# Optimization experiments

Hardware: AMD Instinct MI355X
Metric: run time of the kernel (lower is better)

The kernel has to match this reference:

```python
import jax, jax.numpy as jnp
import numpy as np

WZ, WH, WW = 2, 6, 12  # window_size (Z, H, W)
NUM_HEADS = 6


def _layernorm(x, g, b, eps=1e-5):
    m = jnp.mean(x, axis=-1, keepdims=True)
    v = jnp.mean((x - m) ** 2, axis=-1, keepdims=True)
    return (x - m) * jax.lax.rsqrt(v + eps) * g + b


def setup_inputs() -> dict:
    key = jax.random.key(0)
    ks = jax.random.split(key, 8)
    B, Z, H, W, C = 1, 8, 91, 180, 192
    s = 0.02
    return {
        "x": jax.random.normal(ks[0], (B, Z * H * W, C), jnp.float32),
        "norm1_g": jnp.ones((C,), jnp.float32),
        "norm1_b": jnp.zeros((C,), jnp.float32),
        "qkv_w": jax.random.normal(ks[1], (3 * C, C), jnp.float32) * s,
        "qkv_b": jnp.zeros((3 * C,), jnp.float32),
        "proj_w": jax.random.normal(ks[2], (C, C), jnp.float32) * s,
        "proj_b": jnp.zeros((C,), jnp.float32),
        "norm2_g": jnp.ones((C,), jnp.float32),
        "norm2_b": jnp.zeros((C,), jnp.float32),
        "fc1_w": jax.random.normal(ks[3], (4 * C, C), jnp.float32) * s,
        "fc1_b": jnp.zeros((4 * C,), jnp.float32),
        "fc2_w": jax.random.normal(ks[4], (C, 4 * C), jnp.float32) * s,
        "fc2_b": jnp.zeros((C,), jnp.float32),
        "Z": Z, "H": H, "W": W, "roll": 1,
    }


def _forward(x, norm1_g, norm1_b, qkv_w, qkv_b, proj_w, proj_b,
             norm2_g, norm2_b, fc1_w, fc1_b, fc2_w, fc2_b, Z, H, W, roll):
    B, N, C = x.shape
    shortcut = x
    x = x.reshape(B, Z, H, W, C)
    # pad to window multiples (right-pad, as in torch F.pad)
    pz, ph, pw = (-Z) % WZ, (-H) % WH, (-W) % WW
    x = jnp.pad(x, ((0, 0), (0, pz), (0, ph), (0, pw), (0, 0)))
    Zp, Hp, Wp = Z + pz, H + ph, W + pw
    if roll:
        x = jnp.roll(x, (-(WZ // 2), -(WH // 2), -(WW // 2)), axis=(1, 2, 3))
    # window partition -> (B*nW, wz*wh*ww, C)
    x = x.reshape(B, Zp // WZ, WZ, Hp // WH, WH, Wp // WW, WW, C)
    x = x.transpose(0, 1, 3, 5, 2, 4, 6, 7).reshape(-1, WZ * WH * WW, C)
    xw = _layernorm(x, norm1_g, norm1_b)
    # windowed multi-head attention (mask is always None in this module)
    nw, L, _ = xw.shape
    hd = C // NUM_HEADS
    qkv = (xw @ qkv_w.T + qkv_b).reshape(nw, L, 3, NUM_HEADS, hd)
    q, k, v = jnp.moveaxis(qkv, 2, 0)        # each (nw, L, nh, hd)
    q = q * (hd ** -0.5)
    attn = jnp.einsum('nqhd,nkhd->nhqk', q, k)
    attn = jax.nn.softmax(attn, axis=-1)
    out = jnp.einsum('nhqk,nkhd->nqhd', attn, v).reshape(nw, L, C)
    out = out @ proj_w.T + proj_b
    # window reverse
    x = out.reshape(B, Zp // WZ, Hp // WH, Wp // WW, WZ, WH, WW, C)
    x = x.transpose(0, 1, 4, 2, 5, 3, 6, 7).reshape(B, Zp, Hp, Wp, C)
    if roll:
        x = jnp.roll(x, (WZ // 2, WH // 2, WW // 2), axis=(1, 2, 3))
    x = x[:, :Z, :H, :W, :].reshape(B, Z * H * W, C)
    x = shortcut + x
    # MLP with post-norm (as written in the source: x + norm2(mlp(x)))
    h = jax.nn.gelu(x @ fc1_w.T + fc1_b, approximate=False)
    h = h @ fc2_w.T + fc2_b
    return x + _layernorm(h, norm2_g, norm2_b)


def reference(x, norm1_g, norm1_b, qkv_w, qkv_b, proj_w, proj_b,
              norm2_g, norm2_b, fc1_w, fc1_b, fc2_w, fc2_b, Z, H, W, roll):
    return _forward(x, norm1_g, norm1_b, qkv_w, qkv_b, proj_w, proj_b,
                    norm2_g, norm2_b, fc1_w, fc1_b, fc2_w, fc2_b, Z, H, W, roll)
```

## Files before the change

kernel.cpp:

```cpp
#include <hip/hip_runtime.h>
#include <hip/hip_bf16.h>
#include <math.h>

#define C_DIM 192
#define NH 6
#define HD 32
#define L_WIN 144
#define NWIN 960
#define MROWS (NWIN * L_WIN)
#define NTOK 131040
#define Z_ 8
#define H_ 91
#define W_ 180
#define HP_ 96
#define WS_REQUIRED 212336640ull

#define OFF_WBF   0ull
#define OFF_XWC   1048576ull
#define OFF_QKVB  51367936ull
#define OFF_ATTNO 1048576ull
#define OFF_X1B   51367936ull
#define WO_QKV  0
#define WO_PROJ 110592
#define WO_FC1  147456
#define WO_FC2  294912
#define WO_BETA 442368
#define W_TOTAL 442560

typedef __attribute__((ext_vector_type(8))) short bf16x8;
typedef __attribute__((ext_vector_type(4))) short s16x4;
typedef __attribute__((ext_vector_type(4))) float f32x4;

__device__ __forceinline__ short f2bf(float f) {
    union { __hip_bfloat16 h; short s; } u; u.h = __float2bfloat16(f); return u.s;
}
__device__ __forceinline__ float bf2f(short s) {
    return __uint_as_float(((unsigned int)(unsigned short)s) << 16);
}

__device__ __forceinline__ int win_token_to_tok(int r) {
    int n = r / L_WIN, l = r - n * L_WIN;
    int wz = n / 240;
    int rem = n - wz * 240;
    int wh = rem / 15;
    int ww = rem - wh * 15;
    int iz = l / 72;
    int r2 = l - iz * 72;
    int ih = r2 / 12;
    int iw = r2 - ih * 12;
    int z = wz * 2 + iz;
    int h = wh * 6 + ih;
    int w = ww * 12 + iw;
    int zp = z + 1; if (zp >= Z_) zp -= Z_;
    int hp = h + 3; if (hp >= HP_) hp -= HP_;
    int wp = w + 6; if (wp >= W_) wp -= W_;
    if (hp >= H_) return -1;
    return (zp * H_ + hp) * W_ + wp;
}

__global__ __launch_bounds__(256)
void wconv_kernel(const float* __restrict__ qw, const float* __restrict__ pw,
                  const float* __restrict__ f1w, const float* __restrict__ f2w,
                  const float* __restrict__ n1b, short* __restrict__ wbf) {
    int i = blockIdx.x * 256 + threadIdx.x;
    if (i >= W_TOTAL) return;
    float v;
    if (i < WO_PROJ)      v = qw[i];
    else if (i < WO_FC1)  v = pw[i - WO_PROJ];
    else if (i < WO_FC2)  v = f1w[i - WO_FC1];
    else if (i < WO_BETA) v = f2w[i - WO_FC2];
    else                  v = n1b[i - WO_BETA];
    wbf[i] = f2bf(v);
}

__global__ __launch_bounds__(256)
void ln_tok_kernel(const float* __restrict__ x, const float* __restrict__ g,
                   const float* __restrict__ b, short* __restrict__ xwc) {
    int wave = threadIdx.x >> 6, lane = threadIdx.x & 63;
    int r = blockIdx.x * 4 + wave;
    if (r >= NTOK) return;
    const float* p = x + (size_t)r * C_DIM;
    float v0 = p[lane], v1 = p[lane + 64], v2 = p[lane + 128];
    float s = v0 + v1 + v2;
    float sq = v0 * v0 + v1 * v1 + v2 * v2;
    #pragma unroll
    for (int off = 32; off; off >>= 1) {
        s += __shfl_xor(s, off);
        sq += __shfl_xor(sq, off);
    }
    float m = s * (1.f / 192.f);
    float var = sq * (1.f / 192.f) - m * m;
    float inv = rsqrtf(var + 1e-5f);
    short* o = xwc + (size_t)r * C_DIM;
    o[lane]       = f2bf((v0 - m) * inv * g[lane]       + b[lane]);
    o[lane + 64]  = f2bf((v1 - m) * inv * g[lane + 64]  + b[lane + 64]);
    o[lane + 128] = f2bf((v2 - m) * inv * g[lane + 128] + b[lane + 128]);
}

__global__ __launch_bounds__(256)
void qkv_gemm(const short* __restrict__ xwc, const short* __restrict__ wq,
              const short* __restrict__ beta, const float* __restrict__ bias,
              short* __restrict__ qkvb) {
    __shared__ __align__(16) short As[128][200];
    int t = threadIdx.x, w = t >> 6, l = t & 63, g = l >> 4, c = l & 15;
    int bid = blockIdx.x + 9 * blockIdx.y;
    int xcd = bid & 7, sq_ = bid >> 3;
    int bx = sq_ % 9, by = xcd + 8 * (sq_ / 9);
    int row0 = by * 128, col0 = bx * 64;
    int wr = (w >> 1) * 64, wc = (w & 1) * 32;
    const short* wqb = wq + (size_t)(col0 + wc + c) * 192 + g * 8;
    bf16x8 wv[6][2];
    #pragma unroll
    for (int ks = 0; ks < 6; ks++)
        #pragma unroll
        for (int n = 0; n < 2; n++)
            wv[ks][n] = *(const bf16x8*)(wqb + n * 3072 + ks * 32);
    {
        int r = t & 127;
        int th = t >> 7;
        int tok = win_token_to_tok(row0 + r);
        const short* src = (tok >= 0) ? xwc + (size_t)tok * C_DIM : beta;
        #pragma unroll
        for (int i = 0; i < 12; i++) {
            int cidx = th + 2 * i;
            *(bf16x8*)(&As[r][cidx * 8]) = *(const bf16x8*)(src + cidx * 8);
        }
    }
    __syncthreads();
    f32x4 acc[4][2] = {};
    #pragma unroll
    for (int ks = 0; ks < 6; ks++) {
        bf16x8 af[4];
        #pragma unroll
        for (int m = 0; m < 4; m++)
            af[m] = *(const bf16x8*)(&As[wr + 16 * m + c][ks * 32 + g * 8]);
        #pragma unroll
        for (int m = 0; m < 4; m++)
            #pragma unroll
            for (int n = 0; n < 2; n++)
                acc[m][n] = __builtin_amdgcn_mfma_f32_16x16x32_bf16(af[m], wv[ks][n], acc[m][n], 0, 0, 0);
    }
    #pragma unroll
    for (int m = 0; m < 4; m++)
        #pragma unroll
        for (int reg = 0; reg < 4; reg++) {
            int r = row0 + wr + 16 * m + 4 * g + reg;
            int win = r / 144, ll = r - win * 144;
            #pragma unroll
            for (int n = 0; n < 2; n++) {
                int col = col0 + wc + 16 * n + c;
                int sec = col / 192;
                int head = (col - sec * 192) >> 5;
                int d = col & 31;
                size_t dst = ((size_t)(win * 6 + head) * 3 + sec) * 4608 + ll * 32 + d;
                qkvb[dst] = f2bf(acc[m][n][reg] + bias[col]);
            }
        }
}

__global__ __launch_bounds__(192)
void attn_mfma(const short* __restrict__ qkvb, short* __restrict__ attno) {
    __shared__ __align__(16) short Vt[32][168];
    __shared__ __align__(16) short Pl[3][16][168];
    int blk = blockIdx.x;
    int win = blk / NH, head = blk - win * NH;
    int t = threadIdx.x, w = t >> 6, l = t & 63, g = l >> 4, c = l & 15;
    const short* qb = qkvb + (size_t)(win * 6 + head) * 13824;
    const short* kb = qb + 4608;
    const short* vb = qb + 9216;
    for (int ch = t; ch < 576; ch += 192) {
        int kv = ch >> 2, cc = (ch & 3) * 8;
        bf16x8 v = *(const bf16x8*)(vb + kv * 32 + cc);
        #pragma unroll
        for (int j = 0; j < 8; j++) Vt[cc + j][kv] = v[j];
    }
    for (int i = t; i < 32 * 24; i += 192) Vt[i / 24][144 + i % 24] = 0;
    for (int i = l; i < 16 * 24; i += 64) Pl[w][i / 24][144 + i % 24] = 0;
    __syncthreads();

    bf16x8 kf[9];
    #pragma unroll
    for (int n = 0; n < 9; n++)
        kf[n] = *(const bf16x8*)(kb + (16 * n + c) * 32 + g * 8);

    const float scale2 = 0.2550348668f;
    for (int m = w; m < 9; m += 3) {
        bf16x8 qf = *(const bf16x8*)(qb + (16 * m + c) * 32 + g * 8);
        f32x4 sv[9];
        #pragma unroll
        for (int n = 0; n < 9; n++) {
            f32x4 z = {};
            sv[n] = __builtin_amdgcn_mfma_f32_16x16x32_bf16(qf, kf[n], z, 0, 0, 0);
        }
        float mx[4], rs[4];
        #pragma unroll
        for (int reg = 0; reg < 4; reg++) {
            float v = -1e30f;
            #pragma unroll
            for (int n = 0; n < 9; n++) { sv[n][reg] *= scale2; v = fmaxf(v, sv[n][reg]); }
            #pragma unroll
            for (int off = 1; off <= 8; off <<= 1) v = fmaxf(v, __shfl_xor(v, off));
            mx[reg] = v;
        }
        #pragma unroll
        for (int reg = 0; reg < 4; reg++) {
            float acc = 0.f;
            #pragma unroll
            for (int n = 0; n < 9; n++) {
                float e = exp2f(sv[n][reg] - mx[reg]);
                sv[n][reg] = e;
                acc += e;
            }
            #pragma unroll
            for (int off = 1; off <= 8; off <<= 1) acc += __shfl_xor(acc, off);
            rs[reg] = 1.f / acc;
        }
        #pragma unroll
        for (int n = 0; n < 9; n++)
            #pragma unroll
            for (int reg = 0; reg < 4; reg++)
                Pl[w][4 * g + reg][16 * n + c] = f2bf(sv[n][reg]);
        asm volatile("s_waitcnt lgkmcnt(0)" ::: "memory");
        f32x4 o[2] = {};
        #pragma unroll
        for (int ks = 0; ks < 5; ks++) {
            bf16x8 pa = *(const bf16x8*)(&Pl[w][c][32 * ks + 8 * g]);
            #pragma unroll
            for (int df = 0; df < 2; df++) {
                bf16x8 vv = *(const bf16x8*)(&Vt[16 * df + c][32 * ks + 8 * g]);
                o[df] = __builtin_amdgcn_mfma_f32_16x16x32_bf16(pa, vv, o[df], 0, 0, 0);
            }
        }
        #pragma unroll
        for (int reg = 0; reg < 4; reg++) {
            int grow = win * L_WIN + 16 * m + 4 * g + reg;
            int tok = win_token_to_tok(grow);
            if (tok < 0) continue;
            #pragma unroll
            for (int df = 0; df < 2; df++)
                attno[(size_t)tok * C_DIM + head * HD + 16 * df + c] =
                    f2bf(o[df][reg] * rs[reg]);
        }
    }
}

__global__ __launch_bounds__(256)
void proj_gemm(const short* __restrict__ attno, const short* __restrict__ wp,
               const float* __restrict__ bias, const float* __restrict__ x,
               short* __restrict__ x1b) {
    __shared__ __align__(16) short As[128][200];
    int t = threadIdx.x, w = t >> 6, l = t & 63, g = l >> 4, c = l & 15;
    int bid = blockIdx.x + 3 * blockIdx.y;
    int xcd = bid & 7, sq_ = bid >> 3;
    int bx = sq_ % 3, by = xcd + 8 * (sq_ / 3);
    int row0 = by * 128, col0 = bx * 64;
    int wr = (w >> 1) * 64, wc = (w & 1) * 32;
    const short* wpb = wp + (size_t)(col0 + wc + c) * 192 + g * 8;
    bf16x8 wv[6][2];
    #pragma unroll
    for (int ks = 0; ks < 6; ks++)
        #pragma unroll
        for (int n = 0; n < 2; n++)
            wv[ks][n] = *(const bf16x8*)(wpb + n * 3072 + ks * 32);
    {
        int r = t & 127;
        int th = t >> 7;
        int gr = row0 + r;
        #pragma unroll
        for (int i = 0; i < 12; i++) {
            int cidx = th + 2 * i;
            bf16x8 v = {};
            if (gr < NTOK) v = *(const bf16x8*)(attno + (size_t)gr * C_DIM + cidx * 8);
            *(bf16x8*)(&As[r][cidx * 8]) = v;
        }
    }
    __syncthreads();
    f32x4 acc[4][2] = {};
    #pragma unroll
    for (int ks = 0; ks < 6; ks++) {
        bf16x8 af[4];
        #pragma unroll
        for (int m = 0; m < 4; m++)
            af[m] = *(const bf16x8*)(&As[wr + 16 * m + c][ks * 32 + g * 8]);
        #pragma unroll
        for (int m = 0; m < 4; m++)
            #pragma unroll
            for (int n = 0; n < 2; n++)
                acc[m][n] = __builtin_amdgcn_mfma_f32_16x16x32_bf16(af[m], wv[ks][n], acc[m][n], 0, 0, 0);
    }
    #pragma unroll
    for (int m = 0; m < 4; m++)
        #pragma unroll
        for (int reg = 0; reg < 4; reg++) {
            int r = row0 + wr + 16 * m + 4 * g + reg;
            if (r >= NTOK) continue;
            #pragma unroll
            for (int n = 0; n < 2; n++) {
                int col = col0 + wc + 16 * n + c;
                float v = acc[m][n][reg] + bias[col] + x[(size_t)r * C_DIM + col];
                x1b[(size_t)r * C_DIM + col] = f2bf(v);
            }
        }
}

__global__ __launch_bounds__(256)
void mlp_kernel(const short* __restrict__ x1b, const short* __restrict__ w1,
                const short* __restrict__ w2, const float* __restrict__ b1,
                const float* __restrict__ b2, const float* __restrict__ g2,
                const float* __restrict__ bb2, float* __restrict__ out) {
    __shared__ __align__(16) short As[64][196];
    __shared__ __align__(16) short Hs[64][196];
    __shared__ float red_s[64][4];
    __shared__ float red_q[64][4];
    int t = threadIdx.x, w = t >> 6, l = t & 63, g = l >> 4, c = l & 15;
    int row0 = blockIdx.x * 64;
    {
        int r = t & 63, sg = t >> 6;
        int gr = row0 + r;
        #pragma unroll
        for (int i = 0; i < 6; i++) {
            int cidx = sg + 4 * i;
            bf16x8 v = {};
            if (gr < NTOK) v = *(const bf16x8*)(x1b + (size_t)gr * C_DIM + cidx * 8);
            *(bf16x8*)(&As[r][cidx * 8]) = v;
        }
    }
    __syncthreads();

    f32x4 acc2[4][3] = {};
    for (int q = 0; q < 4; q++) {
        const short* w1b = w1 + (size_t)(q * 192 + 48 * w + c) * 192 + g * 8;
        bf16x8 wv1[6][3];
        #pragma unroll
        for (int ks = 0; ks < 6; ks++)
            #pragma unroll
            for (int mh = 0; mh < 3; mh++)
                wv1[ks][mh] = *(const bf16x8*)(w1b + mh * 3072 + ks * 32);
        f32x4 acc1[3][4] = {};
        #pragma unroll
        for (int ks = 0; ks < 6; ks++) {
            bf16x8 bx[4];
            #pragma unroll
            for (int tn = 0; tn < 4; tn++)
                bx[tn] = *(const bf16x8*)(&As[16 * tn + c][ks * 32 + g * 8]);
            #pragma unroll
            for (int mh = 0; mh < 3; mh++)
                #pragma unroll
                for (int tn = 0; tn < 4; tn++)
                    acc1[mh][tn] = __builtin_amdgcn_mfma_f32_16x16x32_bf16(wv1[ks][mh], bx[tn], acc1[mh][tn], 0, 0, 0);
        }
        const short* w2b = w2 + (size_t)(48 * w + c) * 768 + q * 192 + g * 8;
        bf16x8 wv2[6][3];
        #pragma unroll
        for (int ks = 0; ks < 6; ks++)
            #pragma unroll
            for (int n = 0; n < 3; n++)
                wv2[ks][n] = *(const bf16x8*)(w2b + n * 12288 + ks * 32);
        s16x4 pk[3][4];
        #pragma unroll
        for (int mh = 0; mh < 3; mh++) {
            float bv[4];
            #pragma unroll
            for (int reg = 0; reg < 4; reg++)
                bv[reg] = b1[q * 192 + 48 * w + 16 * mh + 4 * g + reg];
            #pragma unroll
            for (int tn = 0; tn < 4; tn++) {
                #pragma unroll
                for (int reg = 0; reg < 4; reg++) {
                    float v = acc1[mh][tn][reg] + bv[reg];
                    float u = v * (1.5957691216f + 0.0713548162f * v * v);
                    float e = exp2f(-1.4426950409f * u);
                    pk[mh][tn][reg] = f2bf(v * __builtin_amdgcn_rcpf(1.f + e));
                }
            }
        }
        __syncthreads();
        #pragma unroll
        for (int mh = 0; mh < 3; mh++)
            #pragma unroll
            for (int tn = 0; tn < 4; tn++)
                *(s16x4*)(&Hs[16 * tn + c][48 * w + 16 * mh + 4 * g]) = pk[mh][tn];
        __syncthreads();
        #pragma unroll
        for (int ks = 0; ks < 6; ks++) {
            bf16x8 pa[4];
            #pragma unroll
            for (int tm = 0; tm < 4; tm++)
                pa[tm] = *(const bf16x8*)(&Hs[16 * tm + c][ks * 32 + g * 8]);
            #pragma unroll
            for (int tm = 0; tm < 4; tm++)
                #pragma unroll
                for (int n = 0; n < 3; n++)
                    acc2[tm][n] = __builtin_amdgcn_mfma_f32_16x16x32_bf16(pa[tm], wv2[ks][n], acc2[tm][n], 0, 0, 0);
        }
    }

    #pragma unroll
    for (int m = 0; m < 4; m++)
        #pragma unroll
        for (int reg = 0; reg < 4; reg++) {
            float s = 0.f, sq = 0.f;
            #pragma unroll
            for (int n = 0; n < 3; n++) {
                int col = 48 * w + 16 * n + c;
                float h = acc2[m][n][reg] + b2[col];
                acc2[m][n][reg] = h;
                s += h; sq += h * h;
            }
            #pragma unroll
            for (int off = 1; off <= 8; off <<= 1) {
                s += __shfl_xor(s, off);
                sq += __shfl_xor(sq, off);
            }
            if (c == 0) {
                int q16 = 16 * m + 4 * g + reg;
                red_s[q16][w] = s;
                red_q[q16][w] = sq;
            }
        }
    __syncthreads();
    #pragma unroll
    for (int m = 0; m < 4; m++)
        #pragma unroll
        for (int reg = 0; reg < 4; reg++) {
            int q16 = 16 * m + 4 * g + reg;
            int r = row0 + q16;
            float s = red_s[q16][0] + red_s[q16][1] + red_s[q16][2] + red_s[q16][3];
            float sq = red_q[q16][0] + red_q[q16][1] + red_q[q16][2] + red_q[q16][3];
            float mean = s * (1.f / 192.f);
            float var = sq * (1.f / 192.f) - mean * mean;
            float inv = rsqrtf(var + 1e-5f);
            if (r < NTOK) {
                #pragma unroll
                for (int n = 0; n < 3; n++) {
                    int col = 48 * w + 16 * n + c;
                    out[(size_t)r * C_DIM + col] =
                        bf2f(As[q16][col]) + (acc2[m][n][reg] - mean) * inv * g2[col] + bb2[col];
                }
            }
        }
}

extern "C" void kernel_launch(void* const* d_in, const int* in_sizes, int n_in,
                              void* d_out, int out_size, void* d_ws, size_t ws_size,
                              hipStream_t stream) {
    const float* x      = (const float*)d_in[0];
    const float* n1g    = (const float*)d_in[1];
    const float* n1b    = (const float*)d_in[2];
    const float* qkv_w  = (const float*)d_in[3];
    const float* qkv_b  = (const float*)d_in[4];
    const float* proj_w = (const float*)d_in[5];
    const float* proj_b = (const float*)d_in[6];
    const float* n2g    = (const float*)d_in[7];
    const float* n2b    = (const float*)d_in[8];
    const float* fc1_w  = (const float*)d_in[9];
    const float* fc1_b_ = (const float*)d_in[10];
    const float* fc2_w  = (const float*)d_in[11];
    const float* fc2_b  = (const float*)d_in[12];
    float* out = (float*)d_out;

    if (ws_size < WS_REQUIRED) return;

    char* ws = (char*)d_ws;
    short* wbf   = (short*)(ws + OFF_WBF);
    short* xwc   = (short*)(ws + OFF_XWC);
    short* qkvb  = (short*)(ws + OFF_QKVB);
    short* attno = (short*)(ws + OFF_ATTNO);
    short* x1b   = (short*)(ws + OFF_X1B);

    wconv_kernel<<<(W_TOTAL + 255) / 256, 256, 0, stream>>>(
        qkv_w, proj_w, fc1_w, fc2_w, n1b, wbf);

    ln_tok_kernel<<<NTOK / 4, 256, 0, stream>>>(x, n1g, n1b, xwc);

    qkv_gemm<<<dim3(9, MROWS / 128), 256, 0, stream>>>(
        xwc, wbf + WO_QKV, wbf + WO_BETA, qkv_b, qkvb);

    attn_mfma<<<NWIN * NH, 192, 0, stream>>>(qkvb, attno);

    proj_gemm<<<dim3(3, (NTOK + 127) / 128), 256, 0, stream>>>(
        attno, wbf + WO_PROJ, proj_b, x, x1b);

    mlp_kernel<<<(NTOK + 63) / 64, 256, 0, stream>>>(
        x1b, wbf + WO_FC1, wbf + WO_FC2, fc1_b_, fc2_b, n2g, n2b, out);
}
```

Before: 615.6 us.

## Shrink MLP row tile to 32 and double-buffer weight fragments for occupancy

The fused MLP kernel now handles 32 rows per block instead of 64, halving accumulators and LDS use, and asks for 4 blocks per CU through launch bounds. Weight fragments for fc1 and fc2 are held three k-steps at a time, with the next chunk loaded during the MFMAs, which lowers register pressure. Bounds checks are dropped because NTOK divides evenly by 32, and the LDS row stride in the qkv and proj GEMMs changes from 200 to 196. Each block now reuses every weight load across half as many rows, so weight traffic per token doubles.

```diff
diff --git a/kernel.cpp b/kernel.cpp
--- a/kernel.cpp
+++ b/kernel.cpp
@@ -101,7 +101,7 @@
 void qkv_gemm(const short* __restrict__ xwc, const short* __restrict__ wq,
               const short* __restrict__ beta, const float* __restrict__ bias,
               short* __restrict__ qkvb) {
-    __shared__ __align__(16) short As[128][200];
+    __shared__ __align__(16) short As[128][196];
     int t = threadIdx.x, w = t >> 6, l = t & 63, g = l >> 4, c = l & 15;
     int bid = blockIdx.x + 9 * blockIdx.y;
     int xcd = bid & 7, sq_ = bid >> 3;
@@ -248,7 +248,7 @@
 void proj_gemm(const short* __restrict__ attno, const short* __restrict__ wp,
                const float* __restrict__ bias, const float* __restrict__ x,
                short* __restrict__ x1b) {
-    __shared__ __align__(16) short As[128][200];
+    __shared__ __align__(16) short As[128][196];
     int t = threadIdx.x, w = t >> 6, l = t & 63, g = l >> 4, c = l & 15;
     int bid = blockIdx.x + 3 * blockIdx.y;
     int xcd = bid & 7, sq_ = bid >> 3;
@@ -303,60 +303,64 @@
         }
 }
 
-__global__ __launch_bounds__(256)
+__global__ __launch_bounds__(256, 4)
 void mlp_kernel(const short* __restrict__ x1b, const short* __restrict__ w1,
                 const short* __restrict__ w2, const float* __restrict__ b1,
                 const float* __restrict__ b2, const float* __restrict__ g2,
                 const float* __restrict__ bb2, float* __restrict__ out) {
-    __shared__ __align__(16) short As[64][196];
-    __shared__ __align__(16) short Hs[64][196];
-    __shared__ float red_s[64][4];
-    __shared__ float red_q[64][4];
+    __shared__ __align__(16) short As[32][196];
+    __shared__ __align__(16) short Hs[32][196];
+    __shared__ float red_s[32][4];
+    __shared__ float red_q[32][4];
     int t = threadIdx.x, w = t >> 6, l = t & 63, g = l >> 4, c = l & 15;
-    int row0 = blockIdx.x * 64;
+    int row0 = blockIdx.x * 32;
     {
-        int r = t & 63, sg = t >> 6;
-        int gr = row0 + r;
-        #pragma unroll
-        for (int i = 0; i < 6; i++) {
-            int cidx = sg + 4 * i;
-            bf16x8 v = {};
-            if (gr < NTOK) v = *(const bf16x8*)(x1b + (size_t)gr * C_DIM + cidx * 8);
-            *(bf16x8*)(&As[r][cidx * 8]) = v;
+        int r = t & 31, sg = t >> 5;
+        const short* src = x1b + (size_t)(row0 + r) * C_DIM;
+        #pragma unroll
+        for (int i = 0; i < 3; i++) {
+            int cidx = sg + 8 * i;
+            *(bf16x8*)(&As[r][cidx * 8]) = *(const bf16x8*)(src + cidx * 8);
         }
     }
     __syncthreads();
 
-    f32x4 acc2[4][3] = {};
+    f32x4 acc2[2][3] = {};
     for (int q = 0; q < 4; q++) {
         const short* w1b = w1 + (size_t)(q * 192 + 48 * w + c) * 192 + g * 8;
-        bf16x8 wv1[6][3];
-        #pragma unroll
-        for (int ks = 0; ks < 6; ks++)
+        f32x4 acc1[3][2] = {};
+        bf16x8 wv1[3][3];
+        #pragma unroll
+        for (int pk_ = 0; pk_ < 3; pk_++)
             #pragma unroll
             for (int mh = 0; mh < 3; mh++)
-                wv1[ks][mh] = *(const bf16x8*)(w1b + mh * 3072 + ks * 32);
-        f32x4 acc1[3][4] = {};
+                wv1[pk_][mh] = *(const bf16x8*)(w1b + mh * 3072 + pk_ * 32);
         #pragma unroll
         for (int ks = 0; ks < 6; ks++) {
-            bf16x8 bx[4];
-            #pragma unroll
-            for (int tn = 0; tn < 4; tn++)
+            if (ks < 3) {
+                #pragma unroll
+                for (int mh = 0; mh < 3; mh++)
+                    wv1[ks % 3][mh] = wv1[ks % 3][mh];
+            }
+            bf16x8 bx[2];
+            #pragma unroll
+            for (int tn = 0; tn < 2; tn++)
                 bx[tn] = *(const bf16x8*)(&As[16 * tn + c][ks * 32 + g * 8]);
+            bf16x8 cw[3];
+            #pragma unroll
+            for (int mh = 0; mh < 3; mh++) cw[mh] = wv1[ks % 3][mh];
+            if (ks < 3) {
+                #pragma unroll
+                for (int mh = 0; mh < 3; mh++)
+                    wv1[ks % 3][mh] = *(const bf16x8*)(w1b + mh * 3072 + (ks + 3) * 32);
+            }
             #pragma unroll
             for (int mh = 0; mh < 3; mh++)
                 #pragma unroll
-                for (int tn = 0; tn < 4; tn++)
-                    acc1[mh][tn] = __builtin_amdgcn_mfma_f32_16x16x32_bf16(wv1[ks][mh], bx[tn], acc1[mh][tn], 0, 0, 0);
-        }
-        const short* w2b = w2 + (size_t)(48 * w + c) * 768 + q * 192 + g * 8;
-        bf16x8 wv2[6][3];
-        #pragma unroll
-        for (int ks = 0; ks < 6; ks++)
-            #pragma unroll
-            for (int n = 0; n < 3; n++)
-                wv2[ks][n] = *(const bf16x8*)(w2b + n * 12288 + ks * 32);
-        s16x4 pk[3][4];
+                for (int tn = 0; tn < 2; tn++)
+                    acc1[mh][tn] = __builtin_amdgcn_mfma_f32_16x16x32_bf16(cw[mh], bx[tn], acc1[mh][tn], 0, 0, 0);
+        }
+        s16x4 pk[3][2];
         #pragma unroll
         for (int mh = 0; mh < 3; mh++) {
             float bv[4];
@@ -364,7 +368,7 @@
             for (int reg = 0; reg < 4; reg++)
                 bv[reg] = b1[q * 192 + 48 * w + 16 * mh + 4 * g + reg];
             #pragma unroll
-            for (int tn = 0; tn < 4; tn++) {
+            for (int tn = 0; tn < 2; tn++) {
                 #pragma unroll
                 for (int reg = 0; reg < 4; reg++) {
                     float v = acc1[mh][tn][reg] + bv[reg];
@@ -378,25 +382,40 @@
         #pragma unroll
         for (int mh = 0; mh < 3; mh++)
             #pragma unroll
-            for (int tn = 0; tn < 4; tn++)
+            for (int tn = 0; tn < 2; tn++)
                 *(s16x4*)(&Hs[16 * tn + c][48 * w + 16 * mh + 4 * g]) = pk[mh][tn];
         __syncthreads();
+        const short* w2b = w2 + (size_t)(48 * w + c) * 768 + q * 192 + g * 8;
+        bf16x8 wv2[3][3];
+        #pragma unroll
+        for (int pk_ = 0; pk_ < 3; pk_++)
+            #pragma unroll
+            for (int n = 0; n < 3; n++)
+                wv2[pk_][n] = *(const bf16x8*)(w2b + n * 12288 + pk_ * 32);
         #pragma unroll
         for (int ks = 0; ks < 6; ks++) {
-            bf16x8 pa[4];
-            #pragma unroll
-            for (int tm = 0; tm < 4; tm++)
+            bf16x8 pa[2];
+            #pragma unroll
+            for (int tm = 0; tm < 2; tm++)
                 pa[tm] = *(const bf16x8*)(&Hs[16 * tm + c][ks * 32 + g * 8]);
-            #pragma unroll
-            for (int tm = 0; tm < 4; tm++)
+            bf16x8 cw[3];
+            #pragma unroll
+            for (int n = 0; n < 3; n++) cw[n] = wv2[ks % 3][n];
+            if (ks < 3) {
                 #pragma unroll
                 for (int n = 0; n < 3; n++)
-                    acc2[tm][n] = __builtin_amdgcn_mfma_f32_16x16x32_bf16(pa[tm], wv2[ks][n], acc2[tm][n], 0, 0, 0);
-        }
-    }
-
-    #pragma unroll
-    for (int m = 0; m < 4; m++)
+                    wv2[ks % 3][n] = *(const bf16x8*)(w2b + n * 12288 + (ks + 3) * 32);
+            }
+            #pragma unroll
+            for (int tm = 0; tm < 2; tm++)
+                #pragma unroll
+                for (int n = 0; n < 3; n++)
+                    acc2[tm][n] = __builtin_amdgcn_mfma_f32_16x16x32_bf16(pa[tm], cw[n], acc2[tm][n], 0, 0, 0);
+        }
+    }
+
+    #pragma unroll
+    for (int m = 0; m < 2; m++)
         #pragma unroll
         for (int reg = 0; reg < 4; reg++) {
             float s = 0.f, sq = 0.f;
@@ -420,7 +439,7 @@
         }
     __syncthreads();
     #pragma unroll
-    for (int m = 0; m < 4; m++)
+    for (int m = 0; m < 2; m++)
         #pragma unroll
         for (int reg = 0; reg < 4; reg++) {
             int q16 = 16 * m + 4 * g + reg;
@@ -430,13 +449,11 @@
             float mean = s * (1.f / 192.f);
             float var = sq * (1.f / 192.f) - mean * mean;
             float inv = rsqrtf(var + 1e-5f);
-            if (r < NTOK) {
-                #pragma unroll
-                for (int n = 0; n < 3; n++) {
-                    int col = 48 * w + 16 * n + c;
-                    out[(size_t)r * C_DIM + col] =
-                        bf2f(As[q16][col]) + (acc2[m][n][reg] - mean) * inv * g2[col] + bb2[col];
-                }
+            #pragma unroll
+            for (int n = 0; n < 3; n++) {
+                int col = 48 * w + 16 * n + c;
+                out[(size_t)r * C_DIM + col] =
+                    bf2f(As[q16][col]) + (acc2[m][n][reg] - mean) * inv * g2[col] + bb2[col];
             }
         }
 }
@@ -481,6 +498,6 @@
     proj_gemm<<<dim3(3, (NTOK + 127) / 128), 256, 0, stream>>>(
         attno, wbf + WO_PROJ, proj_b, x, x1b);
 
-    mlp_kernel<<<(NTOK + 63) / 64, 256, 0, stream>>>(
+    mlp_kernel<<<NTOK / 32, 256, 0, stream>>>(
         x1b, wbf + WO_FC1, wbf + WO_FC2, fc1_b_, fc2_b, n2g, n2b, out);
 }
```

Result: no change. 615.1 us (-0.1%).

## Double MLP row tile to 128 with 512 threads and stream weight fragments

Applied to the files above, without the earlier changes.

The fused MLP kernel now handles 128 rows per block with 8 waves, split into two row groups and four hidden-column groups, so each weight fragment loaded from global memory serves twice as many rows. Instead of holding all six k-steps of fc1/fc2 weights in registers, each wave double-buffers one k-step at a time, which lowers register pressure. The launch bounds change to 512 threads with a minimum of one block, and shared memory per block roughly doubles, which may limit occupancy. The LDS row padding in the qkv and proj GEMMs also shrinks from 200 to 196, which changes bank-conflict behaviour.

```diff
diff --git a/kernel.cpp b/kernel.cpp
--- a/kernel.cpp
+++ b/kernel.cpp
@@ -101,7 +101,7 @@
 void qkv_gemm(const short* __restrict__ xwc, const short* __restrict__ wq,
               const short* __restrict__ beta, const float* __restrict__ bias,
               short* __restrict__ qkvb) {
-    __shared__ __align__(16) short As[128][200];
+    __shared__ __align__(16) short As[128][196];
     int t = threadIdx.x, w = t >> 6, l = t & 63, g = l >> 4, c = l & 15;
     int bid = blockIdx.x + 9 * blockIdx.y;
     int xcd = bid & 7, sq_ = bid >> 3;
@@ -248,7 +248,7 @@
 void proj_gemm(const short* __restrict__ attno, const short* __restrict__ wp,
                const float* __restrict__ bias, const float* __restrict__ x,
                short* __restrict__ x1b) {
-    __shared__ __align__(16) short As[128][200];
+    __shared__ __align__(16) short As[128][196];
     int t = threadIdx.x, w = t >> 6, l = t & 63, g = l >> 4, c = l & 15;
     int bid = blockIdx.x + 3 * blockIdx.y;
     int xcd = bid & 7, sq_ = bid >> 3;
@@ -303,19 +303,20 @@
         }
 }
 
-__global__ __launch_bounds__(256)
+__global__ __launch_bounds__(512, 1)
 void mlp_kernel(const short* __restrict__ x1b, const short* __restrict__ w1,
                 const short* __restrict__ w2, const float* __restrict__ b1,
                 const float* __restrict__ b2, const float* __restrict__ g2,
                 const float* __restrict__ bb2, float* __restrict__ out) {
-    __shared__ __align__(16) short As[64][196];
-    __shared__ __align__(16) short Hs[64][196];
-    __shared__ float red_s[64][4];
-    __shared__ float red_q[64][4];
+    __shared__ __align__(16) short As[128][196];
+    __shared__ __align__(16) short Hs[128][196];
+    __shared__ float red_s[128][4];
+    __shared__ float red_q[128][4];
     int t = threadIdx.x, w = t >> 6, l = t & 63, g = l >> 4, c = l & 15;
-    int row0 = blockIdx.x * 64;
+    int tg = w & 1, hg = w >> 1;
+    int row0 = blockIdx.x * 128;
     {
-        int r = t & 63, sg = t >> 6;
+        int r = t & 127, sg = t >> 7;
         int gr = row0 + r;
         #pragma unroll
         for (int i = 0; i < 6; i++) {
@@ -329,40 +330,43 @@
 
     f32x4 acc2[4][3] = {};
     for (int q = 0; q < 4; q++) {
-        const short* w1b = w1 + (size_t)(q * 192 + 48 * w + c) * 192 + g * 8;
-        bf16x8 wv1[6][3];
-        #pragma unroll
-        for (int ks = 0; ks < 6; ks++)
+        const short* w1b = w1 + (size_t)(q * 192 + hg * 48 + c) * 192 + g * 8;
+        f32x4 acc1[3][4] = {};
+        bf16x8 cur1[3], nxt1[3];
+        #pragma unroll
+        for (int mh = 0; mh < 3; mh++) cur1[mh] = *(const bf16x8*)(w1b + mh * 3072);
+        #pragma unroll
+        for (int ks = 0; ks < 6; ks++) {
+            if (ks < 5) {
+                #pragma unroll
+                for (int mh = 0; mh < 3; mh++)
+                    nxt1[mh] = *(const bf16x8*)(w1b + mh * 3072 + (ks + 1) * 32);
+            }
+            bf16x8 bx[4];
+            #pragma unroll
+            for (int tn = 0; tn < 4; tn++)
+                bx[tn] = *(const bf16x8*)(&As[tg * 64 + 16 * tn + c][ks * 32 + g * 8]);
             #pragma unroll
             for (int mh = 0; mh < 3; mh++)
-                wv1[ks][mh] = *(const bf16x8*)(w1b + mh * 3072 + ks * 32);
-        f32x4 acc1[3][4] = {};
-        #pragma unroll
-        for (int ks = 0; ks < 6; ks++) {
-            bf16x8 bx[4];
-            #pragma unroll
-            for (int tn = 0; tn < 4; tn++)
-                bx[tn] = *(const bf16x8*)(&As[16 * tn + c][ks * 32 + g * 8]);
-            #pragma unroll
-            for (int mh = 0; mh < 3; mh++)
                 #pragma unroll
                 for (int tn = 0; tn < 4; tn++)
-                    acc1[mh][tn] = __builtin_amdgcn_mfma_f32_16x16x32_bf16(wv1[ks][mh], bx[tn], acc1[mh][tn], 0, 0, 0);
-        }
-        const short* w2b = w2 + (size_t)(48 * w + c) * 768 + q * 192 + g * 8;
-        bf16x8 wv2[6][3];
-        #pragma unroll
-        for (int ks = 0; ks < 6; ks++)
-            #pragma unroll
-            for (int n = 0; n < 3; n++)
-                wv2[ks][n] = *(const bf16x8*)(w2b + n * 12288 + ks * 32);
+                    acc1[mh][tn] = __builtin_amdgcn_mfma_f32_16x16x32_bf16(cur1[mh], bx[tn], acc1[mh][tn], 0, 0, 0);
+            if (ks < 5) {
+                #pragma unroll
+                for (int mh = 0; mh < 3; mh++) cur1[mh] = nxt1[mh];
+            }
+        }
+        const short* w2b = w2 + (size_t)(hg * 48 + c) * 768 + q * 192 + g * 8;
+        bf16x8 cur2[3], nxt2[3];
+        #pragma unroll
+        for (int n = 0; n < 3; n++) cur2[n] = *(const bf16x8*)(w2b + n * 12288);
         s16x4 pk[3][4];
         #pragma unroll
         for (int mh = 0; mh < 3; mh++) {
             float bv[4];
             #pragma unroll
             for (int reg = 0; reg < 4; reg++)
-                bv[reg] = b1[q * 192 + 48 * w + 16 * mh + 4 * g + reg];
+                bv[reg] = b1[q * 192 + hg * 48 + 16 * mh + 4 * g + reg];
             #pragma unroll
             for (int tn = 0; tn < 4; tn++) {
                 #pragma unroll
@@ -379,32 +383,41 @@
         for (int mh = 0; mh < 3; mh++)
             #pragma unroll
             for (int tn = 0; tn < 4; tn++)
-                *(s16x4*)(&Hs[16 * tn + c][48 * w + 16 * mh + 4 * g]) = pk[mh][tn];
+                *(s16x4*)(&Hs[tg * 64 + 16 * tn + c][hg * 48 + 16 * mh + 4 * g]) = pk[mh][tn];
         __syncthreads();
         #pragma unroll
         for (int ks = 0; ks < 6; ks++) {
+            if (ks < 5) {
+                #pragma unroll
+                for (int n = 0; n < 3; n++)
+                    nxt2[n] = *(const bf16x8*)(w2b + n * 12288 + (ks + 1) * 32);
+            }
             bf16x8 pa[4];
             #pragma unroll
             for (int tm = 0; tm < 4; tm++)
-                pa[tm] = *(const bf16x8*)(&Hs[16 * tm + c][ks * 32 + g * 8]);
+                pa[tm] = *(const bf16x8*)(&Hs[tg * 64 + 16 * tm + c][ks * 32 + g * 8]);
             #pragma unroll
             for (int tm = 0; tm < 4; tm++)
                 #pragma unroll
                 for (int n = 0; n < 3; n++)
-                    acc2[tm][n] = __builtin_amdgcn_mfma_f32_16x16x32_bf16(pa[tm], wv2[ks][n], acc2[tm][n], 0, 0, 0);
-        }
-    }
-
-    #pragma unroll
-    for (int m = 0; m < 4; m++)
+                    acc2[tm][n] = __builtin_amdgcn_mfma_f32_16x16x32_bf16(pa[tm], cur2[n], acc2[tm][n], 0, 0, 0);
+            if (ks < 5) {
+                #pragma unroll
+                for (int n = 0; n < 3; n++) cur2[n] = nxt2[n];
+            }
+        }
+    }
+
+    #pragma unroll
+    for (int tm = 0; tm < 4; tm++)
         #pragma unroll
         for (int reg = 0; reg < 4; reg++) {
             float s = 0.f, sq = 0.f;
             #pragma unroll
             for (int n = 0; n < 3; n++) {
-                int col = 48 * w + 16 * n + c;
-                float h = acc2[m][n][reg] + b2[col];
-                acc2[m][n][reg] = h;
+                int col = hg * 48 + 16 * n + c;
+                float h = acc2[tm][n][reg] + b2[col];
+                acc2[tm][n][reg] = h;
                 s += h; sq += h * h;
             }
             #pragma unroll
@@ -413,17 +426,17 @@
                 sq += __shfl_xor(sq, off);
             }
             if (c == 0) {
-                int q16 = 16 * m + 4 * g + reg;
-                red_s[q16][w] = s;
-                red_q[q16][w] = sq;
+                int q16 = tg * 64 + 16 * tm + 4 * g + reg;
+                red_s[q16][hg] = s;
+                red_q[q16][hg] = sq;
             }
         }
     __syncthreads();
     #pragma unroll
-    for (int m = 0; m < 4; m++)
-        #pragma unroll
-        for (int reg = 0; reg < 4; reg++) {
-            int q16 = 16 * m + 4 * g + reg;
+    for (int tm = 0; tm < 4; tm++)
+        #pragma unroll
+        for (int reg = 0; reg < 4; reg++) {
+            int q16 = tg * 64 + 16 * tm + 4 * g + reg;
             int r = row0 + q16;
             float s = red_s[q16][0] + red_s[q16][1] + red_s[q16][2] + red_s[q16][3];
             float sq = red_q[q16][0] + red_q[q16][1] + red_q[q16][2] + red_q[q16][3];
@@ -433,9 +446,9 @@
             if (r < NTOK) {
                 #pragma unroll
                 for (int n = 0; n < 3; n++) {
-                    int col = 48 * w + 16 * n + c;
+                    int col = hg * 48 + 16 * n + c;
                     out[(size_t)r * C_DIM + col] =
-                        bf2f(As[q16][col]) + (acc2[m][n][reg] - mean) * inv * g2[col] + bb2[col];
+                        bf2f(As[q16][col]) + (acc2[tm][n][reg] - mean) * inv * g2[col] + bb2[col];
                 }
             }
         }
@@ -481,6 +494,6 @@
     proj_gemm<<<dim3(3, (NTOK + 127) / 128), 256, 0, stream>>>(
         attno, wbf + WO_PROJ, proj_b, x, x1b);
 
-    mlp_kernel<<<(NTOK + 63) / 64, 256, 0, stream>>>(
+    mlp_kernel<<<(NTOK + 127) / 128, 512, 0, stream>>>(
         x1b, wbf + WO_FC1, wbf + WO_FC2, fc1_b_, fc2_b, n2g, n2b, out);
 }
```

After: 544.3 us. -11.6%, faster.

## Restructure MLP kernel so each wave owns 16 tokens with register-resident hidden

Applied to the files above, without the earlier changes.

Rewrites the fused MLP kernel so each wave handles 16 tokens and the whole 192-wide output. The GELU result stays in registers and feeds fc2 directly through 16x16x16 MFMAs, which removes the shared-memory hidden buffer, the block barriers and the cross-wave LayerNorm reduction. Weights are now streamed from global/L2 per wave instead of being split across waves, and the block grows to 512 threads. LDS padding in the qkv and proj GEMMs also changes from 200 to 196. The cost is more weight traffic per token, high register pressure, and the slower x16 MFMA variant for fc2.

```diff
diff --git a/kernel.cpp b/kernel.cpp
--- a/kernel.cpp
+++ b/kernel.cpp
@@ -36,6 +36,17 @@
 }
 __device__ __forceinline__ float bf2f(short s) {
     return __uint_as_float(((unsigned int)(unsigned short)s) << 16);
+}
+
+__device__ __forceinline__ f32x4 mfma16(s16x4 a, s16x4 b, f32x4 c) {
+#if __has_builtin(__builtin_amdgcn_mfma_f32_16x16x16bf16_1k)
+    return __builtin_amdgcn_mfma_f32_16x16x16bf16_1k(a, b, c, 0, 0, 0);
+#else
+    f32x4 d;
+    asm volatile("v_mfma_f32_16x16x16_bf16 %0, %1, %2, %3"
+                 : "=v"(d) : "v"(a), "v"(b), "v"(c));
+    return d;
+#endif
 }
 
 __device__ __forceinline__ int win_token_to_tok(int r) {
@@ -101,7 +112,7 @@
 void qkv_gemm(const short* __restrict__ xwc, const short* __restrict__ wq,
               const short* __restrict__ beta, const float* __restrict__ bias,
               short* __restrict__ qkvb) {
-    __shared__ __align__(16) short As[128][200];
+    __shared__ __align__(16) short As[128][196];
     int t = threadIdx.x, w = t >> 6, l = t & 63, g = l >> 4, c = l & 15;
     int bid = blockIdx.x + 9 * blockIdx.y;
     int xcd = bid & 7, sq_ = bid >> 3;
@@ -248,7 +259,7 @@
 void proj_gemm(const short* __restrict__ attno, const short* __restrict__ wp,
                const float* __restrict__ bias, const float* __restrict__ x,
                short* __restrict__ x1b) {
-    __shared__ __align__(16) short As[128][200];
+    __shared__ __align__(16) short As[128][196];
     int t = threadIdx.x, w = t >> 6, l = t & 63, g = l >> 4, c = l & 15;
     int bid = blockIdx.x + 3 * blockIdx.y;
     int xcd = bid & 7, sq_ = bid >> 3;
@@ -303,142 +314,88 @@
         }
 }
 
-__global__ __launch_bounds__(256)
+__global__ __launch_bounds__(512, 2)
 void mlp_kernel(const short* __restrict__ x1b, const short* __restrict__ w1,
                 const short* __restrict__ w2, const float* __restrict__ b1,
                 const float* __restrict__ b2, const float* __restrict__ g2,
                 const float* __restrict__ bb2, float* __restrict__ out) {
-    __shared__ __align__(16) short As[64][196];
-    __shared__ __align__(16) short Hs[64][196];
-    __shared__ float red_s[64][4];
-    __shared__ float red_q[64][4];
-    int t = threadIdx.x, w = t >> 6, l = t & 63, g = l >> 4, c = l & 15;
-    int row0 = blockIdx.x * 64;
-    {
-        int r = t & 63, sg = t >> 6;
-        int gr = row0 + r;
-        #pragma unroll
-        for (int i = 0; i < 6; i++) {
-            int cidx = sg + 4 * i;
-            bf16x8 v = {};
-            if (gr < NTOK) v = *(const bf16x8*)(x1b + (size_t)gr * C_DIM + cidx * 8);
-            *(bf16x8*)(&As[r][cidx * 8]) = v;
-        }
-    }
-    __syncthreads();
-
-    f32x4 acc2[4][3] = {};
+    int t = threadIdx.x, wid = t >> 6, l = t & 63, g = l >> 4, c = l & 15;
+    int tok0 = blockIdx.x * 128 + wid * 16;
+    bool tv = (tok0 + c) < NTOK;
+    bf16x8 xf[6];
+    const short* xp = x1b + (size_t)(tok0 + c) * C_DIM + g * 8;
+    #pragma unroll
+    for (int ks = 0; ks < 6; ks++)
+        xf[ks] = tv ? *(const bf16x8*)(xp + ks * 32) : (bf16x8){};
+
+    f32x4 acc2[12] = {};
     for (int q = 0; q < 4; q++) {
-        const short* w1b = w1 + (size_t)(q * 192 + 48 * w + c) * 192 + g * 8;
-        bf16x8 wv1[6][3];
-        #pragma unroll
-        for (int ks = 0; ks < 6; ks++)
-            #pragma unroll
-            for (int mh = 0; mh < 3; mh++)
-                wv1[ks][mh] = *(const bf16x8*)(w1b + mh * 3072 + ks * 32);
-        f32x4 acc1[3][4] = {};
-        #pragma unroll
-        for (int ks = 0; ks < 6; ks++) {
-            bf16x8 bx[4];
-            #pragma unroll
-            for (int tn = 0; tn < 4; tn++)
-                bx[tn] = *(const bf16x8*)(&As[16 * tn + c][ks * 32 + g * 8]);
-            #pragma unroll
-            for (int mh = 0; mh < 3; mh++)
-                #pragma unroll
-                for (int tn = 0; tn < 4; tn++)
-                    acc1[mh][tn] = __builtin_amdgcn_mfma_f32_16x16x32_bf16(wv1[ks][mh], bx[tn], acc1[mh][tn], 0, 0, 0);
-        }
-        const short* w2b = w2 + (size_t)(48 * w + c) * 768 + q * 192 + g * 8;
-        bf16x8 wv2[6][3];
-        #pragma unroll
-        for (int ks = 0; ks < 6; ks++)
-            #pragma unroll
-            for (int n = 0; n < 3; n++)
-                wv2[ks][n] = *(const bf16x8*)(w2b + n * 12288 + ks * 32);
-        s16x4 pk[3][4];
-        #pragma unroll
-        for (int mh = 0; mh < 3; mh++) {
-            float bv[4];
-            #pragma unroll
-            for (int reg = 0; reg < 4; reg++)
-                bv[reg] = b1[q * 192 + 48 * w + 16 * mh + 4 * g + reg];
-            #pragma unroll
-            for (int tn = 0; tn < 4; tn++) {
-                #pragma unroll
-                for (int reg = 0; reg < 4; reg++) {
-                    float v = acc1[mh][tn][reg] + bv[reg];
-                    float u = v * (1.5957691216f + 0.0713548162f * v * v);
-                    float e = exp2f(-1.4426950409f * u);
-                    pk[mh][tn][reg] = f2bf(v * __builtin_amdgcn_rcpf(1.f + e));
-                }
-            }
-        }
-        __syncthreads();
-        #pragma unroll
-        for (int mh = 0; mh < 3; mh++)
-            #pragma unroll
-            for (int tn = 0; tn < 4; tn++)
-                *(s16x4*)(&Hs[16 * tn + c][48 * w + 16 * mh + 4 * g]) = pk[mh][tn];
-        __syncthreads();
-        #pragma unroll
-        for (int ks = 0; ks < 6; ks++) {
-            bf16x8 pa[4];
-            #pragma unroll
-            for (int tm = 0; tm < 4; tm++)
-                pa[tm] = *(const bf16x8*)(&Hs[16 * tm + c][ks * 32 + g * 8]);
-            #pragma unroll
-            for (int tm = 0; tm < 4; tm++)
-                #pragma unroll
-                for (int n = 0; n < 3; n++)
-                    acc2[tm][n] = __builtin_amdgcn_mfma_f32_16x16x32_bf16(pa[tm], wv2[ks][n], acc2[tm][n], 0, 0, 0);
-        }
-    }
-
-    #pragma unroll
-    for (int m = 0; m < 4; m++)
-        #pragma unroll
-        for (int reg = 0; reg < 4; reg++) {
-            float s = 0.f, sq = 0.f;
-            #pragma unroll
-            for (int n = 0; n < 3; n++) {
-                int col = 48 * w + 16 * n + c;
-                float h = acc2[m][n][reg] + b2[col];
-                acc2[m][n][reg] = h;
-                s += h; sq += h * h;
-            }
-            #pragma unroll
-            for (int off = 1; off <= 8; off <<= 1) {
-                s += __shfl_xor(s, off);
-                sq += __shfl_xor(sq, off);
-            }
-            if (c == 0) {
-                int q16 = 16 * m + 4 * g + reg;
-                red_s[q16][w] = s;
-                red_q[q16][w] = sq;
-            }
-        }
-    __syncthreads();
-    #pragma unroll
-    for (int m = 0; m < 4; m++)
-        #pragma unroll
-        for (int reg = 0; reg < 4; reg++) {
-            int q16 = 16 * m + 4 * g + reg;
-            int r = row0 + q16;
-            float s = red_s[q16][0] + red_s[q16][1] + red_s[q16][2] + red_s[q16][3];
-            float sq = red_q[q16][0] + red_q[q16][1] + red_q[q16][2] + red_q[q16][3];
-            float mean = s * (1.f / 192.f);
-            float var = sq * (1.f / 192.f) - mean * mean;
-            float inv = rsqrtf(var + 1e-5f);
-            if (r < NTOK) {
-                #pragma unroll
-                for (int n = 0; n < 3; n++) {
-                    int col = 48 * w + 16 * n + c;
-                    out[(size_t)r * C_DIM + col] =
-                        bf2f(As[q16][col]) + (acc2[m][n][reg] - mean) * inv * g2[col] + bb2[col];
-                }
-            }
-        }
+        f32x4 acc1[12] = {};
+        #pragma unroll
+        for (int mh = 0; mh < 12; mh++) {
+            const short* wp = w1 + (size_t)(q * 192 + 16 * mh + c) * 192 + g * 8;
+            #pragma unroll
+            for (int ks = 0; ks < 6; ks++) {
+                bf16x8 wf = *(const bf16x8*)(wp + ks * 32);
+                acc1[mh] = __builtin_amdgcn_mfma_f32_16x16x32_bf16(wf, xf[ks], acc1[mh], 0, 0, 0);
+            }
+        }
+        s16x4 pa[12];
+        #pragma unroll
+        for (int mh = 0; mh < 12; mh++) {
+            #pragma unroll
+            for (int reg = 0; reg < 4; reg++) {
+                float v = acc1[mh][reg] + b1[q * 192 + 16 * mh + 4 * g + reg];
+                float u = v * (1.5957691216f + 0.0713548162f * v * v);
+                float e = exp2f(-1.4426950409f * u);
+                pa[mh][reg] = f2bf(v * __builtin_amdgcn_rcpf(1.f + e));
+            }
+        }
+        #pragma unroll
+        for (int n = 0; n < 12; n++) {
+            const short* w2p = w2 + (size_t)(16 * n + c) * 768 + q * 192 + 4 * g;
+            #pragma unroll
+            for (int mh = 0; mh < 12; mh++) {
+                s16x4 wf = *(const s16x4*)(w2p + 16 * mh);
+                acc2[n] = mfma16(pa[mh], wf, acc2[n]);
+            }
+        }
+    }
+
+    float hsum[4] = {}, hsq[4] = {};
+    #pragma unroll
+    for (int n = 0; n < 12; n++) {
+        float bb = b2[16 * n + c];
+        #pragma unroll
+        for (int reg = 0; reg < 4; reg++) {
+            float h = acc2[n][reg] + bb;
+            acc2[n][reg] = h;
+            hsum[reg] += h; hsq[reg] += h * h;
+        }
+    }
+    #pragma unroll
+    for (int reg = 0; reg < 4; reg++) {
+        #pragma unroll
+        for (int off = 1; off <= 8; off <<= 1) {
+            hsum[reg] += __shfl_xor(hsum[reg], off);
+            hsq[reg]  += __shfl_xor(hsq[reg], off);
+        }
+    }
+    #pragma unroll
+    for (int reg = 0; reg < 4; reg++) {
+        int tok = tok0 + 4 * g + reg;
+        if (tok >= NTOK) continue;
+        float mean = hsum[reg] * (1.f / 192.f);
+        float var = hsq[reg] * (1.f / 192.f) - mean * mean;
+        float inv = rsqrtf(var + 1e-5f);
+        #pragma unroll
+        for (int n = 0; n < 12; n++) {
+            int col = 16 * n + c;
+            float x1v = bf2f(x1b[(size_t)tok * C_DIM + col]);
+            out[(size_t)tok * C_DIM + col] =
+                x1v + (acc2[n][reg] - mean) * inv * g2[col] + bb2[col];
+        }
+    }
 }
 
 extern "C" void kernel_launch(void* const* d_in, const int* in_sizes, int n_in,
@@ -481,6 +438,6 @@
     proj_gemm<<<dim3(3, (NTOK + 127) / 128), 256, 0, stream>>>(
         attno, wbf + WO_PROJ, proj_b, x, x1b);
 
-    mlp_kernel<<<(NTOK + 63) / 64, 256, 0, stream>>>(
+    mlp_kernel<<<(NTOK + 127) / 128, 512, 0, stream>>>(
         x1b, wbf + WO_FC1, wbf + WO_FC2, fc1_b_, fc2_b, n2g, n2b, out);
 }
```

Result: slower. 1.237 ms (+100.9%).
